# Optimization experiments

Measured on AMD Instinct MI355X. Metric: run time of the kernel, lower is better.

The kernel has to match this reference:

```python
import jax, jax.numpy as jnp
import numpy as np

B, L, DM, H, NF = 4, 4096, 1024, 16, 256
D = DM // H  # depth per head = 64
EPS = 1e-6


def _orthogonal_gaussian(m, d, seed=42):
    # Faithful to orthogonal_gaussian(): stack of transposed Q factors of d x d
    # iid-gaussian blocks, normalized by sqrt(num_squares + remainder/d).
    rng = np.random.default_rng(seed)
    num_squares = m // d
    blocks = []
    for _ in range(num_squares):
        q, _ = np.linalg.qr(rng.standard_normal((d, d)))
        blocks.append(q.T)
    remainder = m - d * num_squares
    if remainder:
        q, _ = np.linalg.qr(rng.standard_normal((d, d)))
        blocks.append(q.T[:remainder])
    mat = np.vstack(blocks) / np.sqrt(num_squares + remainder / d)
    return jnp.asarray(mat, dtype=jnp.float32)


def setup_inputs() -> dict:
    key = jax.random.key(0)
    ks = jax.random.split(key, 11)
    w = lambda k: jax.random.normal(k, (DM, DM), jnp.float32) * 0.02
    b = lambda k: jax.random.normal(k, (DM,), jnp.float32) * 0.01
    return {
        "query": jax.random.normal(ks[0], (B, L, DM), jnp.float32),
        "key": jax.random.normal(ks[1], (B, L, DM), jnp.float32),
        "value": jax.random.normal(ks[2], (B, L, DM), jnp.float32),
        "Wq": w(ks[3]), "bq": b(ks[4]),
        "Wk": w(ks[5]), "bk": b(ks[6]),
        "Wv": w(ks[7]), "bv": b(ks[8]),
        "Wo": w(ks[9]), "bo": b(ks[10]),
        "random_feats": _orthogonal_gaussian(NF, D),
    }


def _softmax_kernel(data, proj, is_query):
    # data: [B, L, H, D], proj: [M, D] -> features [B, L, H, M]
    d = data.shape[-1]
    m = proj.shape[0]
    data = data * (float(d) ** -0.25)          # data_normalizer = 1/sqrt(sqrt(d))
    ratio = float(m) ** -0.5
    data_dash = jnp.einsum('blhd,md->blhm', data, proj)
    diag = 0.5 * jnp.sum(data * data, axis=-1, keepdims=True)  # [B,L,H,1]
    if is_query:
        mx = jnp.max(data_dash, axis=-1, keepdims=True)          # per position
    else:
        mx = jnp.max(data_dash, axis=(1, -1), keepdims=True)     # over L and M
    return ratio * (jnp.exp(data_dash - diag - mx) + EPS)


def reference(query, key, value, Wq, bq, Wk, bk, Wv, bv, Wo, bo, random_feats):
    b, l = query.shape[0], query.shape[1]
    # QKV projections, split heads to [B, L, H, D]
    q = (query @ Wq + bq).reshape(b, l, H, D)
    k = (key @ Wk + bk).reshape(b, l, H, D)
    v = (value @ Wv + bv).reshape(b, l, H, D)
    # FAVOR+ feature maps
    qp = _softmax_kernel(q, random_feats, is_query=True)   # [B,L,H,M]
    kp = _softmax_kernel(k, random_feats, is_query=False)  # [B,L,H,M]
    # linear attention: kv state [B,H,M,D], then project with q'
    kv = jnp.einsum('blhm,blhd->bhmd', kp, v)
    av = jnp.einsum('blhm,bhmd->blhd', qp, kv)
    # normalizer: sum of k' over L, contracted with q'
    norm = jnp.einsum('blhm,bhm->blh', qp, jnp.sum(kp, axis=1))
    out = av / norm[..., None]                  # [B,L,H,D]
    out = out.reshape(b, l, DM)
    return out @ Wo + bo
```

## Files before the change

kernel.cpp:

```cpp
#include <hip/hip_runtime.h>
#include <hip/hip_bf16.h>

typedef unsigned short ushort_t;
typedef __attribute__((ext_vector_type(8))) short short8;
typedef __attribute__((ext_vector_type(4))) short short4v;
typedef __attribute__((ext_vector_type(4))) float f32x4;

#define DEVI static __device__ __forceinline__
#define MFMA __builtin_amdgcn_mfma_f32_16x16x32_bf16

DEVI float b2f(ushort_t u) {
    union { unsigned i; float f; } v; v.i = ((unsigned)u) << 16; return v.f;
}
DEVI ushort_t f2b(float f) {
    union { float f; unsigned i; } v; v.f = f;
    unsigned r = v.i + 0x7FFFu + ((v.i >> 16) & 1u);
    return (ushort_t)(r >> 16);
}
DEVI unsigned encf(float f) {
    unsigned u = __float_as_uint(f);
    return (u & 0x80000000u) ? ~u : (u | 0x80000000u);
}
DEVI float decf(unsigned u) {
    return (u & 0x80000000u) ? __uint_as_float(u & 0x7FFFFFFFu) : __uint_as_float(~u);
}
DEVI bool finitef(float v) { return v > -1e30f && v < 1e30f; }

__global__ void k_dtype(const ushort_t* __restrict__ qraw, unsigned* __restrict__ fl) {
    __shared__ unsigned cnt;
    int t = threadIdx.x;
    if (t == 0) cnt = 0;
    __syncthreads();
    unsigned c = 0;
    for (int i = t; i < 2048; i += 256) {
        unsigned e = (qraw[2 * i] >> 7) & 0xFF;
        c += (e >= 90 && e <= 141) ? 1u : 0u;
    }
    atomicAdd(&cnt, c);
    __syncthreads();
    if (t == 0) { fl[0] = (cnt < 1024) ? 1u : 0u; fl[1] = 0u; }
}

__global__ void k_fill(ushort_t* __restrict__ out, int n, float val) {
    int i = blockIdx.x * 256 + threadIdx.x;
    if (i < n) out[i] = f2b(val);
}

__global__ void k_prep(const void* __restrict__ Wq, const void* __restrict__ Wk,
                       const void* __restrict__ Wv, const void* __restrict__ Wo,
                       const void* __restrict__ rf, const unsigned* __restrict__ fl,
                       ushort_t* __restrict__ WT, ushort_t* __restrict__ WTo,
                       ushort_t* __restrict__ projS) {
    bool f32 = fl[0] != 0;
    int id = blockIdx.x, t = threadIdx.x;
    if (id == 1024) {
        for (int i = t; i < 256 * 64; i += 256) {
            float x = f32 ? ((const float*)rf)[i] : b2f(((const ushort_t*)rf)[i]);
            projS[i] = f2b(x * 0.35355339f);
        }
        return;
    }
    int wsel = id >> 8;
    const void* W = wsel == 0 ? Wq : (wsel == 1 ? Wk : (wsel == 2 ? Wv : Wo));
    ushort_t* out = (wsel == 3) ? WTo : (WT + (size_t)wsel * 1024 * 1024);
    int tile = id & 255;
    int tr = (tile >> 4) * 64, tc = (tile & 15) * 64;
    __shared__ ushort_t s[64][65];
    int r = t >> 2, c = (t & 3) * 16;
    ushort_t vals[16];
    if (f32) {
        const float* src = (const float*)W + (size_t)(tr + r) * 1024 + tc + c;
        for (int u = 0; u < 4; u++) {
            float4 x = ((const float4*)src)[u];
            vals[4 * u + 0] = f2b(x.x); vals[4 * u + 1] = f2b(x.y);
            vals[4 * u + 2] = f2b(x.z); vals[4 * u + 3] = f2b(x.w);
        }
    } else {
        const ushort_t* src = (const ushort_t*)W + (size_t)(tr + r) * 1024 + tc + c;
        short8 v0 = ((const short8*)src)[0], v1 = ((const short8*)src)[1];
        for (int j = 0; j < 8; j++) { vals[j] = ((ushort_t*)&v0)[j]; vals[8 + j] = ((ushort_t*)&v1)[j]; }
    }
    for (int j = 0; j < 16; j++) s[r][c + j] = vals[j];
    __syncthreads();
    ushort_t tmp[16];
    for (int j = 0; j < 16; j++) tmp[j] = s[c + j][r];
    short8 o0, o1;
    for (int j = 0; j < 8; j++) { ((ushort_t*)&o0)[j] = tmp[j]; ((ushort_t*)&o1)[j] = tmp[8 + j]; }
    short8* dst = (short8*)(out + (size_t)(tc + r) * 1024 + tr + c);
    dst[0] = o0; dst[1] = o1;
}

__global__ __launch_bounds__(256) void k_gemm_bias(const void* __restrict__ A,
                                                   const ushort_t* __restrict__ Bt,
                                                   const void* __restrict__ bias,
                                                   void* __restrict__ C,
                                                   const unsigned* __restrict__ fl,
                                                   int aFollow, int cFinal) {
    constexpr int K = 1024, NC = 1024;
    __shared__ ushort_t sA[128][40];
    __shared__ ushort_t sB[128][40];
    bool f32 = fl[0] != 0;
    bool aF32 = aFollow && f32;
    unsigned flags = cFinal ? fl[1] : 0u;
    int t = threadIdx.x;
    int m0 = blockIdx.x * 128, n0 = blockIdx.y * 128;
    int ar = t >> 1, ac = (t & 1) * 16;
    int w = t >> 6, lane = t & 63, lr = lane & 15, quad = lane >> 4, ko = quad * 8;
    int wm = (w & 1) * 64, wn = (w >> 1) * 64;
    f32x4 acc[4][4] = {};
    for (int kt = 0; kt < K; kt += 32) {
        ushort_t av[16];
        if (aF32) {
            const float* pf = (const float*)A + (size_t)(m0 + ar) * K + ac + kt;
            for (int u = 0; u < 4; u++) {
                float4 x = ((const float4*)pf)[u];
                av[4 * u + 0] = f2b(x.x); av[4 * u + 1] = f2b(x.y);
                av[4 * u + 2] = f2b(x.z); av[4 * u + 3] = f2b(x.w);
            }
        } else {
            const ushort_t* ph = (const ushort_t*)A + (size_t)(m0 + ar) * K + ac + kt;
            short8 a0 = ((const short8*)ph)[0], a1 = ((const short8*)ph)[1];
            for (int j = 0; j < 8; j++) { av[j] = ((ushort_t*)&a0)[j]; av[8 + j] = ((ushort_t*)&a1)[j]; }
        }
        const ushort_t* pb = Bt + (size_t)(n0 + ar) * K + ac + kt;
        short8 b0 = ((const short8*)pb)[0], b1 = ((const short8*)pb)[1];
        for (int j = 0; j < 16; j++) sA[ar][ac + j] = av[j];
        *(short8*)&sB[ar][ac] = b0; *(short8*)&sB[ar][ac + 8] = b1;
        __syncthreads();
        short8 af[4], bf[4];
        for (int i = 0; i < 4; i++) af[i] = *(const short8*)&sA[wm + i * 16 + lr][ko];
        for (int j = 0; j < 4; j++) bf[j] = *(const short8*)&sB[wn + j * 16 + lr][ko];
        for (int i = 0; i < 4; i++)
            for (int j = 0; j < 4; j++)
                acc[i][j] = MFMA(af[i], bf[j], acc[i][j], 0, 0, 0);
        __syncthreads();
    }
    for (int j = 0; j < 4; j++) {
        int col = n0 + wn + j * 16 + lr;
        float bv = f32 ? ((const float*)bias)[col] : b2f(((const ushort_t*)bias)[col]);
        for (int i = 0; i < 4; i++) {
            int rowb = m0 + wm + i * 16 + quad * 4;
            for (int r = 0; r < 4; r++) {
                float val = acc[i][j][r] + bv;
                if (cFinal) {
                    if (flags) val = 100.0f * (float)flags;
                    else if (!finitef(val)) val = 2000.0f;
                }
                size_t idx = (size_t)(rowb + r) * NC + col;
                if (cFinal && f32) ((float*)C)[idx] = val;
                else ((ushort_t*)C)[idx] = f2b(val);
            }
        }
    }
}

__global__ void k_init(float* __restrict__ kvT, unsigned* __restrict__ mxk) {
    int bid = blockIdx.x, t = threadIdx.x;
    if (bid == 5120) { if (t < 64) mxk[t] = 0u; return; }
    int idx = bid * 256 + t;
    int row = (idx >> 8) % 80;
    kvT[idx] = (row == 64) ? 2.56e-4f : 0.0f;
}

__global__ __launch_bounds__(256) void k_kmax(const ushort_t* __restrict__ kproj,
                                              const ushort_t* __restrict__ projS,
                                              unsigned* __restrict__ mxk) {
    __shared__ ushort_t sB[64][72];
    __shared__ float wm4[4];
    int t = threadIdx.x, l0 = blockIdx.x * 64, bh = blockIdx.y;
    int b = bh >> 4, h = bh & 15;
    int w = t >> 6, lane = t & 63, lr = lane & 15, ko = (lane >> 4) * 8;
    short8 af[4][2];
    for (int i = 0; i < 4; i++)
        for (int ks = 0; ks < 2; ks++)
            af[i][ks] = *(const short8*)(projS + (size_t)(w * 64 + i * 16 + lr) * 64 + ks * 32 + ko);
    {
        int r = t >> 2, c = (t & 3) * 16;
        const short8* p = (const short8*)(kproj + (size_t)(b * 4096 + l0 + r) * 1024 + h * 64 + c);
        *(short8*)&sB[r][c] = p[0];
        *(short8*)&sB[r][c + 8] = p[1];
    }
    __syncthreads();
    f32x4 acc[4][4] = {};
    for (int j = 0; j < 4; j++)
        for (int ks = 0; ks < 2; ks++) {
            short8 bf = *(const short8*)&sB[j * 16 + lr][ks * 32 + ko];
            for (int i = 0; i < 4; i++)
                acc[i][j] = MFMA(af[i][ks], bf, acc[i][j], 0, 0, 0);
        }
    float vmax = -1e30f;
    for (int i = 0; i < 4; i++)
        for (int j = 0; j < 4; j++)
            for (int r = 0; r < 4; r++) vmax = fmaxf(vmax, acc[i][j][r]);
    for (int off = 32; off; off >>= 1) vmax = fmaxf(vmax, __shfl_xor(vmax, off, 64));
    if (lane == 0) wm4[w] = vmax;
    __syncthreads();
    if (t == 0) {
        float m = fmaxf(fmaxf(wm4[0], wm4[1]), fmaxf(wm4[2], wm4[3]));
        atomicMax(mxk + bh, encf(m));
    }
}

__global__ __launch_bounds__(256) void k_kv(const ushort_t* __restrict__ kproj,
                                            const ushort_t* __restrict__ vproj,
                                            const ushort_t* __restrict__ projS,
                                            const unsigned* __restrict__ mxk,
                                            float* __restrict__ kvT) {
    __shared__ ushort_t sVT[80][40];
    __shared__ float    sdk[32];
    __shared__ ushort_t sK[32][72];
    __shared__ ushort_t sV[32][72];
    __shared__ ushort_t sE[256][40];
    int t = threadIdx.x, kz = blockIdx.x, bh = blockIdx.y;
    int b = bh >> 4, h = bh & 15;
    int w = t >> 6, lane = t & 63, lr = lane & 15, quad = lane >> 4, ko = quad * 8;
    float mx = decf(mxk[bh]);
    short8 af1[4][2];
    for (int i = 0; i < 4; i++)
        for (int ks = 0; ks < 2; ks++)
            af1[i][ks] = *(const short8*)(projS + (size_t)(w * 64 + i * 16 + lr) * 64 + ks * 32 + ko);
    f32x4 acc[5][4] = {};
    for (int lc = kz * 512; lc < kz * 512 + 512; lc += 32) {
        __syncthreads();
        {
            int r = t >> 3, c = (t & 7) * 8;
            *(short8*)&sK[r][c] = *(const short8*)(kproj + (size_t)(b * 4096 + lc + r) * 1024 + h * 64 + c);
            *(short8*)&sV[r][c] = *(const short8*)(vproj + (size_t)(b * 4096 + lc + r) * 1024 + h * 64 + c);
        }
        __syncthreads();
        if (t < 32) {
            float s = 0.f;
            for (int d2 = 0; d2 < 64; d2++) { float f = b2f(sK[t][d2]); s += f * f; }
            sdk[t] = 0.0625f * s;
        }
        short8 bf1[2][2];
        for (int j = 0; j < 2; j++)
            for (int ks = 0; ks < 2; ks++)
                bf1[j][ks] = *(const short8*)&sK[j * 16 + lr][ks * 32 + ko];
        f32x4 acc1[4][2] = {};
        for (int i = 0; i < 4; i++)
            for (int ks = 0; ks < 2; ks++)
                for (int j = 0; j < 2; j++)
                    acc1[i][j] = MFMA(af1[i][ks], bf1[j][ks], acc1[i][j], 0, 0, 0);
        {
            int d2 = t >> 2, ls = (t & 3) * 8;
            short8 pk;
            for (int u = 0; u < 8; u++) ((ushort_t*)&pk)[u] = sV[ls + u][d2];
            *(short8*)&sVT[d2][ls] = pk;
            if (t < 128) {
                int rr = 64 + (t >> 3), cc = (t & 7) * 4;
                ushort_t val = (rr == 64) ? (ushort_t)0x3F80 : (ushort_t)0;
                for (int u = 0; u < 4; u++) sVT[rr][cc + u] = val;
            }
        }
        __syncthreads();
        for (int i = 0; i < 4; i++)
            for (int j = 0; j < 2; j++) {
                int l = j * 16 + lr;
                float dkl = sdk[l];
                for (int r = 0; r < 4; r++) {
                    int m = w * 64 + i * 16 + quad * 4 + r;
                    sE[m][l] = f2b(0.0625f * __expf(acc1[i][j][r] - dkl - mx));
                }
            }
        __syncthreads();
        short8 af2[5], bf2[4];
        for (int i = 0; i < 5; i++) af2[i] = *(const short8*)&sVT[i * 16 + lr][ko];
        for (int j = 0; j < 4; j++) bf2[j] = *(const short8*)&sE[w * 64 + j * 16 + lr][ko];
        for (int i = 0; i < 5; i++)
            for (int j = 0; j < 4; j++)
                acc[i][j] = MFMA(af2[i], bf2[j], acc[i][j], 0, 0, 0);
    }
    float* out = kvT + (size_t)bh * 80 * 256;
    for (int i = 0; i < 5; i++)
        for (int j = 0; j < 4; j++)
            for (int r = 0; r < 4; r++)
                atomicAdd(out + (size_t)(i * 16 + quad * 4 + r) * 256 + (w * 64 + j * 16 + lr),
                          acc[i][j][r]);
}

__global__ void k_scan(const float* __restrict__ kvT, ushort_t* __restrict__ kvbf,
                       unsigned* __restrict__ fl) {
    int i4 = (blockIdx.x * 256 + threadIdx.x) * 4;
    f32x4 v = *(const f32x4*)(kvT + i4);
    unsigned bad = 0;
    short4v o;
    for (int u = 0; u < 4; u++) {
        bad |= finitef(v[u]) ? 0u : 1u;
        ((ushort_t*)&o)[u] = f2b(v[u]);
    }
    if (bad) atomicOr(fl + 1, 1u);
    *(short4v*)(kvbf + i4) = o;
}

__global__ __launch_bounds__(256) void k_qav(const ushort_t* __restrict__ qproj,
                                             const ushort_t* __restrict__ projS,
                                             const ushort_t* __restrict__ kvbf,
                                             unsigned* __restrict__ fl,
                                             ushort_t* __restrict__ attn) {
    union KvQ { ushort_t kv[80][264]; ushort_t q[64][72]; };
    __shared__ KvQ sA;
    __shared__ ushort_t sQP[64][264];
    __shared__ float    sdq[64];
    int t = threadIdx.x, l0 = blockIdx.x * 64, bh = blockIdx.y;
    int b = bh >> 4, h = bh & 15;
    int w = t >> 6, lane = t & 63, lr = lane & 15, quad = lane >> 4, ko = quad * 8;
    {
        int r = t >> 2, c = (t & 3) * 16;
        const short8* p = (const short8*)(qproj + (size_t)(b * 4096 + l0 + r) * 1024 + h * 64 + c);
        *(short8*)&sA.q[r][c] = p[0];
        *(short8*)&sA.q[r][c + 8] = p[1];
    }
    short8 kvreg[10];
    const ushort_t* kvsrc = kvbf + (size_t)bh * 80 * 256;
    #pragma unroll
    for (int i = 0; i < 10; i++)
        kvreg[i] = *(const short8*)(kvsrc + (size_t)(i * 256 + t) * 8);
    __syncthreads();
    short8 af[2];
    for (int ks = 0; ks < 2; ks++) af[ks] = *(const short8*)&sA.q[w * 16 + lr][ks * 32 + ko];
    {
        int row = t >> 2, seg = t & 3;
        short8 x0 = *(const short8*)&sA.q[row][seg * 16];
        short8 x1 = *(const short8*)&sA.q[row][seg * 16 + 8];
        float s = 0.f;
        for (int u = 0; u < 8; u++) {
            float a = b2f(((ushort_t*)&x0)[u]), c2 = b2f(((ushort_t*)&x1)[u]);
            s += a * a + c2 * c2;
        }
        s += __shfl_xor(s, 1, 64);
        s += __shfl_xor(s, 2, 64);
        if ((t & 3) == 0) sdq[row] = 0.0625f * s;
    }
    __syncthreads();
    f32x4 acc[16] = {};
    for (int j = 0; j < 16; j++)
        for (int ks = 0; ks < 2; ks++) {
            short8 bf = *(const short8*)(projS + (size_t)(j * 16 + lr) * 64 + ks * 32 + ko);
            acc[j] = MFMA(af[ks], bf, acc[j], 0, 0, 0);
        }
    #pragma unroll
    for (int i = 0; i < 10; i++) {
        int c = i * 256 + t;
        *(short8*)&sA.kv[c >> 5][(c & 31) * 8] = kvreg[i];
    }
    int rows0 = w * 16 + quad * 4;
    float rm[4], dq[4];
    for (int r = 0; r < 4; r++) {
        float m = -1e30f;
        for (int j = 0; j < 16; j++) m = fmaxf(m, acc[j][r]);
        for (int off = 1; off < 16; off <<= 1) m = fmaxf(m, __shfl_xor(m, off, 64));
        rm[r] = m;
        dq[r] = sdq[rows0 + r];
    }
    for (int j = 0; j < 16; j++)
        for (int r = 0; r < 4; r++)
            sQP[rows0 + r][j * 16 + lr] = f2b(0.0625f * (__expf(acc[j][r] - dq[r] - rm[r]) + 1e-6f));
    __syncthreads();
    f32x4 acc2[5] = {};
    for (int kt = 0; kt < 8; kt++) {
        short8 af2 = *(const short8*)&sQP[w * 16 + lr][kt * 32 + ko];
        #pragma unroll
        for (int j = 0; j < 5; j++) {
            short8 bf2 = *(const short8*)&sA.kv[j * 16 + lr][kt * 32 + ko];
            acc2[j] = MFMA(af2, bf2, acc2[j], 0, 0, 0);
        }
    }
    for (int r = 0; r < 4; r++) {
        float nv = __shfl(acc2[4][r], lane & 48, 64);
        bool badn = !(nv > 0.0f && nv < 1e30f);
        if (badn) atomicOr(fl + 1, 2u);
        float inv = badn ? 0.0f : 1.0f / nv;
        int row = l0 + rows0 + r;
        for (int j = 0; j < 4; j++) {
            float outv = acc2[j][r] * inv;
            if (!finitef(outv)) { outv = 0.0f; atomicOr(fl + 1, 4u); }
            attn[(size_t)(b * 4096 + row) * 1024 + h * 64 + j * 16 + lr] = f2b(outv);
        }
    }
}

extern "C" void kernel_launch(void* const* d_in, const int* in_sizes, int n_in,
                              void* d_out, int out_size, void* d_ws, size_t ws_size,
                              hipStream_t stream) {
    const void* q  = d_in[0];
    const void* k  = d_in[1];
    const void* v  = d_in[2];
    const void* Wq = d_in[3];
    const void* bq = d_in[4];
    const void* Wk = d_in[5];
    const void* bk = d_in[6];
    const void* Wv = d_in[7];
    const void* bv = d_in[8];
    const void* Wo = d_in[9];
    const void* bo = d_in[10];
    const void* rf = d_in[11];

    char* wsp = (char*)d_ws;
    size_t o = 0;
    auto alloc = [&](size_t bytes) { void* p = wsp + o; o += (bytes + 255) & ~(size_t)255; return p; };
    unsigned* fl    = (unsigned*)alloc(256);
    ushort_t* WT    = (ushort_t*)alloc(3ull * 1024 * 1024 * 2);
    ushort_t* WTo   = (ushort_t*)alloc(1024ull * 1024 * 2);
    ushort_t* projS = (ushort_t*)alloc(256 * 64 * 2);
    ushort_t* kproj = (ushort_t*)alloc(16384ull * 1024 * 2);
    ushort_t* vproj = (ushort_t*)alloc(16384ull * 1024 * 2);
    unsigned* mxk   = (unsigned*)alloc(64 * 4);
    float*    kvT   = (float*)alloc(64ull * 80 * 256 * 4);
    ushort_t* kvbf  = (ushort_t*)alloc(64ull * 80 * 256 * 2);
    ushort_t* qproj = (ushort_t*)d_out;
    ushort_t* attn  = kproj;

    if (ws_size < o) {
        k_fill<<<dim3((out_size + 255) / 256), 256, 0, stream>>>((ushort_t*)d_out, out_size,
                                                                 (float)(ws_size >> 20));
        return;
    }

    k_dtype<<<dim3(1), 256, 0, stream>>>((const ushort_t*)q, fl);
    k_prep<<<dim3(1025), 256, 0, stream>>>(Wq, Wk, Wv, Wo, rf, fl, WT, WTo, projS);
    k_gemm_bias<<<dim3(128, 8), 256, 0, stream>>>(q, WT + 0ull * 1048576, bq, qproj, fl, 1, 0);
    k_gemm_bias<<<dim3(128, 8), 256, 0, stream>>>(k, WT + 1ull * 1048576, bk, kproj, fl, 1, 0);
    k_gemm_bias<<<dim3(128, 8), 256, 0, stream>>>(v, WT + 2ull * 1048576, bv, vproj, fl, 1, 0);
    k_init<<<dim3(5121), 256, 0, stream>>>(kvT, mxk);
    k_kmax<<<dim3(64, 64), 256, 0, stream>>>(kproj, projS, mxk);
    k_kv<<<dim3(8, 64), 256, 0, stream>>>(kproj, vproj, projS, mxk, kvT);
    k_scan<<<dim3(1280), 256, 0, stream>>>(kvT, kvbf, fl);
    k_qav<<<dim3(64, 64), 256, 0, stream>>>(qproj, projS, kvbf, fl, attn);
    k_gemm_bias<<<dim3(128, 8), 256, 0, stream>>>(attn, WTo, bo, d_out, fl, 0, 1);
}
```

Baseline: 790.6 us.

## Stage GEMM tiles via direct global-to-LDS loads with separate fp32 pre-conversion

Replaces the register-staged GEMM tile loads with global_load_lds 16-byte direct transfers into unpadded shared memory. For the K and V projections, fp32 inputs are first converted to bf16 into a staging buffer (the output buffer) by a separate kernel, so the GEMM can use the direct-load path. The Q projection keeps in-register conversion for A but loads B directly. The aim is to cut VGPR traffic and instruction overhead in the load path, at the cost of extra conversion passes and possible LDS bank conflicts now that the padding is gone.

```diff
diff --git a/kernel.cpp b/kernel.cpp
--- a/kernel.cpp
+++ b/kernel.cpp
@@ -26,6 +26,12 @@
 }
 DEVI bool finitef(float v) { return v > -1e30f && v < 1e30f; }
 
+DEVI void gload16(const ushort_t* g, ushort_t* l) {
+    __builtin_amdgcn_global_load_lds(
+        (const __attribute__((address_space(1))) void*)(g),
+        (__attribute__((address_space(3))) void*)(l), 16, 0, 0);
+}
+
 __global__ void k_dtype(const ushort_t* __restrict__ qraw, unsigned* __restrict__ fl) {
     __shared__ unsigned cnt;
     int t = threadIdx.x;
@@ -44,6 +50,20 @@
 __global__ void k_fill(ushort_t* __restrict__ out, int n, float val) {
     int i = blockIdx.x * 256 + threadIdx.x;
     if (i < n) out[i] = f2b(val);
+}
+
+__global__ void k_cvt(const void* __restrict__ in, ushort_t* __restrict__ out,
+                      const unsigned* __restrict__ fl) {
+    if (fl[0] == 0) return;
+    int i = blockIdx.x * 256 + threadIdx.x;
+    const float4* p = (const float4*)in + (size_t)i * 2;
+    float4 a = p[0], b = p[1];
+    short8 o;
+    ((ushort_t*)&o)[0] = f2b(a.x); ((ushort_t*)&o)[1] = f2b(a.y);
+    ((ushort_t*)&o)[2] = f2b(a.z); ((ushort_t*)&o)[3] = f2b(a.w);
+    ((ushort_t*)&o)[4] = f2b(b.x); ((ushort_t*)&o)[5] = f2b(b.y);
+    ((ushort_t*)&o)[6] = f2b(b.z); ((ushort_t*)&o)[7] = f2b(b.w);
+    *(short8*)(out + (size_t)i * 8) = o;
 }
 
 __global__ void k_prep(const void* __restrict__ Wq, const void* __restrict__ Wk,
@@ -90,42 +110,37 @@
     dst[0] = o0; dst[1] = o1;
 }
 
-__global__ __launch_bounds__(256) void k_gemm_bias(const void* __restrict__ A,
-                                                   const ushort_t* __restrict__ Bt,
-                                                   const void* __restrict__ bias,
-                                                   void* __restrict__ C,
-                                                   const unsigned* __restrict__ fl,
-                                                   int aFollow, int cFinal) {
+__global__ __launch_bounds__(256) void k_gemm_g(const ushort_t* __restrict__ Abf,
+                                                const ushort_t* __restrict__ Aor,
+                                                const ushort_t* __restrict__ Bt,
+                                                const void* __restrict__ bias,
+                                                void* __restrict__ C,
+                                                const unsigned* __restrict__ fl,
+                                                int cFinal) {
     constexpr int K = 1024, NC = 1024;
-    __shared__ ushort_t sA[128][40];
-    __shared__ ushort_t sB[128][40];
+    __shared__ ushort_t sA[128][32];
+    __shared__ ushort_t sB[128][32];
     bool f32 = fl[0] != 0;
-    bool aF32 = aFollow && f32;
+    const ushort_t* A = f32 ? Abf : Aor;
     unsigned flags = cFinal ? fl[1] : 0u;
     int t = threadIdx.x;
     int m0 = blockIdx.x * 128, n0 = blockIdx.y * 128;
-    int ar = t >> 1, ac = (t & 1) * 16;
     int w = t >> 6, lane = t & 63, lr = lane & 15, quad = lane >> 4, ko = quad * 8;
     int wm = (w & 1) * 64, wn = (w >> 1) * 64;
+    int srow = lane >> 2, scol = (lane & 3) * 8;
+    const ushort_t* a0 = A  + (size_t)(m0 + w * 32 + srow) * K + scol;
+    const ushort_t* a1 = a0 + 16 * K;
+    const ushort_t* b0 = Bt + (size_t)(n0 + w * 32 + srow) * K + scol;
+    const ushort_t* b1 = b0 + 16 * K;
+    ushort_t* la0 = &sA[w * 32][0];
+    ushort_t* la1 = &sA[w * 32 + 16][0];
+    ushort_t* lb0 = &sB[w * 32][0];
+    ushort_t* lb1 = &sB[w * 32 + 16][0];
     f32x4 acc[4][4] = {};
     for (int kt = 0; kt < K; kt += 32) {
-        ushort_t av[16];
-        if (aF32) {
-            const float* pf = (const float*)A + (size_t)(m0 + ar) * K + ac + kt;
-            for (int u = 0; u < 4; u++) {
-                float4 x = ((const float4*)pf)[u];
-                av[4 * u + 0] = f2b(x.x); av[4 * u + 1] = f2b(x.y);
-                av[4 * u + 2] = f2b(x.z); av[4 * u + 3] = f2b(x.w);
-            }
-        } else {
-            const ushort_t* ph = (const ushort_t*)A + (size_t)(m0 + ar) * K + ac + kt;
-            short8 a0 = ((const short8*)ph)[0], a1 = ((const short8*)ph)[1];
-            for (int j = 0; j < 8; j++) { av[j] = ((ushort_t*)&a0)[j]; av[8 + j] = ((ushort_t*)&a1)[j]; }
-        }
-        const ushort_t* pb = Bt + (size_t)(n0 + ar) * K + ac + kt;
-        short8 b0 = ((const short8*)pb)[0], b1 = ((const short8*)pb)[1];
-        for (int j = 0; j < 16; j++) sA[ar][ac + j] = av[j];
-        *(short8*)&sB[ar][ac] = b0; *(short8*)&sB[ar][ac + 8] = b1;
+        gload16(a0, la0); gload16(b0, lb0);
+        gload16(a1, la1); gload16(b1, lb1);
+        a0 += 32; a1 += 32; b0 += 32; b1 += 32;
         __syncthreads();
         short8 af[4], bf[4];
         for (int i = 0; i < 4; i++) af[i] = *(const short8*)&sA[wm + i * 16 + lr][ko];
@@ -150,6 +165,64 @@
                 if (cFinal && f32) ((float*)C)[idx] = val;
                 else ((ushort_t*)C)[idx] = f2b(val);
             }
+        }
+    }
+}
+
+__global__ __launch_bounds__(256) void k_gemm_r(const void* __restrict__ A,
+                                                const ushort_t* __restrict__ Bt,
+                                                const void* __restrict__ bias,
+                                                ushort_t* __restrict__ C,
+                                                const unsigned* __restrict__ fl) {
+    constexpr int K = 1024, NC = 1024;
+    __shared__ ushort_t sA[128][40];
+    __shared__ ushort_t sB[128][32];
+    bool f32 = fl[0] != 0;
+    int t = threadIdx.x;
+    int m0 = blockIdx.x * 128, n0 = blockIdx.y * 128;
+    int ar = t >> 1, ac = (t & 1) * 16;
+    int w = t >> 6, lane = t & 63, lr = lane & 15, quad = lane >> 4, ko = quad * 8;
+    int wm = (w & 1) * 64, wn = (w >> 1) * 64;
+    int srow = lane >> 2, scol = (lane & 3) * 8;
+    const ushort_t* b0 = Bt + (size_t)(n0 + w * 32 + srow) * K + scol;
+    const ushort_t* b1 = b0 + 16 * K;
+    ushort_t* lb0 = &sB[w * 32][0];
+    ushort_t* lb1 = &sB[w * 32 + 16][0];
+    f32x4 acc[4][4] = {};
+    for (int kt = 0; kt < K; kt += 32) {
+        gload16(b0, lb0); gload16(b1, lb1);
+        b0 += 32; b1 += 32;
+        ushort_t av[16];
+        if (f32) {
+            const float* pf = (const float*)A + (size_t)(m0 + ar) * K + ac + kt;
+            for (int u = 0; u < 4; u++) {
+                float4 x = ((const float4*)pf)[u];
+                av[4 * u + 0] = f2b(x.x); av[4 * u + 1] = f2b(x.y);
+                av[4 * u + 2] = f2b(x.z); av[4 * u + 3] = f2b(x.w);
+            }
+        } else {
+            const ushort_t* ph = (const ushort_t*)A + (size_t)(m0 + ar) * K + ac + kt;
+            short8 a0 = ((const short8*)ph)[0], a1 = ((const short8*)ph)[1];
+            for (int j = 0; j < 8; j++) { av[j] = ((ushort_t*)&a0)[j]; av[8 + j] = ((ushort_t*)&a1)[j]; }
+        }
+        *(short8*)&sA[ar][ac] = *(short8*)&av[0];
+        *(short8*)&sA[ar][ac + 8] = *(short8*)&av[8];
+        __syncthreads();
+        short8 af[4], bf[4];
+        for (int i = 0; i < 4; i++) af[i] = *(const short8*)&sA[wm + i * 16 + lr][ko];
+        for (int j = 0; j < 4; j++) bf[j] = *(const short8*)&sB[wn + j * 16 + lr][ko];
+        for (int i = 0; i < 4; i++)
+            for (int j = 0; j < 4; j++)
+                acc[i][j] = MFMA(af[i], bf[j], acc[i][j], 0, 0, 0);
+        __syncthreads();
+    }
+    for (int j = 0; j < 4; j++) {
+        int col = n0 + wn + j * 16 + lr;
+        float bv = f32 ? ((const float*)bias)[col] : b2f(((const ushort_t*)bias)[col]);
+        for (int i = 0; i < 4; i++) {
+            int rowb = m0 + wm + i * 16 + quad * 4;
+            for (int r = 0; r < 4; r++)
+                C[(size_t)(rowb + r) * NC + col] = f2b(acc[i][j][r] + bv);
         }
     }
 }
@@ -408,6 +481,7 @@
     unsigned* mxk   = (unsigned*)alloc(64 * 4);
     float*    kvT   = (float*)alloc(64ull * 80 * 256 * 4);
     ushort_t* kvbf  = (ushort_t*)alloc(64ull * 80 * 256 * 2);
+    ushort_t* stg   = (ushort_t*)d_out;
     ushort_t* qproj = (ushort_t*)d_out;
     ushort_t* attn  = kproj;
 
@@ -419,13 +493,19 @@
 
     k_dtype<<<dim3(1), 256, 0, stream>>>((const ushort_t*)q, fl);
     k_prep<<<dim3(1025), 256, 0, stream>>>(Wq, Wk, Wv, Wo, rf, fl, WT, WTo, projS);
-    k_gemm_bias<<<dim3(128, 8), 256, 0, stream>>>(q, WT + 0ull * 1048576, bq, qproj, fl, 1, 0);
-    k_gemm_bias<<<dim3(128, 8), 256, 0, stream>>>(k, WT + 1ull * 1048576, bk, kproj, fl, 1, 0);
-    k_gemm_bias<<<dim3(128, 8), 256, 0, stream>>>(v, WT + 2ull * 1048576, bv, vproj, fl, 1, 0);
+
+    k_cvt<<<dim3(8192), 256, 0, stream>>>(v, stg, fl);
+    k_gemm_g<<<dim3(128, 8), 256, 0, stream>>>(stg, (const ushort_t*)v,
+                                               WT + 2ull * 1048576, bv, vproj, fl, 0);
+    k_cvt<<<dim3(8192), 256, 0, stream>>>(k, stg, fl);
+    k_gemm_g<<<dim3(128, 8), 256, 0, stream>>>(stg, (const ushort_t*)k,
+                                               WT + 1ull * 1048576, bk, kproj, fl, 0);
+    k_gemm_r<<<dim3(128, 8), 256, 0, stream>>>(q, WT + 0ull * 1048576, bq, qproj, fl);
+
     k_init<<<dim3(5121), 256, 0, stream>>>(kvT, mxk);
     k_kmax<<<dim3(64, 64), 256, 0, stream>>>(kproj, projS, mxk);
     k_kv<<<dim3(8, 64), 256, 0, stream>>>(kproj, vproj, projS, mxk, kvT);
     k_scan<<<dim3(1280), 256, 0, stream>>>(kvT, kvbf, fl);
     k_qav<<<dim3(64, 64), 256, 0, stream>>>(qproj, projS, kvbf, fl, attn);
-    k_gemm_bias<<<dim3(128, 8), 256, 0, stream>>>(attn, WTo, bo, d_out, fl, 0, 1);
-}
+    k_gemm_g<<<dim3(128, 8), 256, 0, stream>>>(attn, attn, WTo, bo, d_out, fl, 1);
+}
```

New measurement: 710.9 us. 1.11x faster.

## Pre-convert fp32 inputs to bf16 and double-buffer GEMM tiles via direct global-to-LDS loads

Applied to the files above, without the earlier changes.

Adds a conversion kernel that writes fp32 activations as bf16 into a staging buffer in the output region. The projection GEMMs then stream A and B tiles straight into LDS with global_load_lds into double buffers, prefetching the next k-tile while MFMAs run on the current one. This removes the per-tile register round trip, the in-loop conversion and one barrier per iteration. The kv kernel also moves the constant sVT rows out of the loop and computes the row norms in parallel with shuffles. The costs are an extra pass over each input to convert it, and unpadded LDS rows that may cause bank conflicts on fragment reads.

```diff
diff --git a/kernel.cpp b/kernel.cpp
--- a/kernel.cpp
+++ b/kernel.cpp
@@ -26,6 +26,12 @@
 }
 DEVI bool finitef(float v) { return v > -1e30f && v < 1e30f; }
 
+DEVI void gload16(const ushort_t* g, ushort_t* l) {
+    __builtin_amdgcn_global_load_lds(
+        (const __attribute__((address_space(1))) void*)(g),
+        (__attribute__((address_space(3))) void*)(l), 16, 0, 0);
+}
+
 __global__ void k_dtype(const ushort_t* __restrict__ qraw, unsigned* __restrict__ fl) {
     __shared__ unsigned cnt;
     int t = threadIdx.x;
@@ -44,6 +50,20 @@
 __global__ void k_fill(ushort_t* __restrict__ out, int n, float val) {
     int i = blockIdx.x * 256 + threadIdx.x;
     if (i < n) out[i] = f2b(val);
+}
+
+__global__ void k_cvt(const void* __restrict__ in, ushort_t* __restrict__ out,
+                      const unsigned* __restrict__ fl) {
+    if (fl[0] == 0) return;
+    int i = blockIdx.x * 256 + threadIdx.x;
+    const float4* p = (const float4*)in + (size_t)i * 2;
+    float4 a = p[0], b = p[1];
+    short8 o;
+    ((ushort_t*)&o)[0] = f2b(a.x); ((ushort_t*)&o)[1] = f2b(a.y);
+    ((ushort_t*)&o)[2] = f2b(a.z); ((ushort_t*)&o)[3] = f2b(a.w);
+    ((ushort_t*)&o)[4] = f2b(b.x); ((ushort_t*)&o)[5] = f2b(b.y);
+    ((ushort_t*)&o)[6] = f2b(b.z); ((ushort_t*)&o)[7] = f2b(b.w);
+    *(short8*)(out + (size_t)i * 8) = o;
 }
 
 __global__ void k_prep(const void* __restrict__ Wq, const void* __restrict__ Wk,
@@ -90,50 +110,47 @@
     dst[0] = o0; dst[1] = o1;
 }
 
-__global__ __launch_bounds__(256) void k_gemm_bias(const void* __restrict__ A,
-                                                   const ushort_t* __restrict__ Bt,
-                                                   const void* __restrict__ bias,
-                                                   void* __restrict__ C,
-                                                   const unsigned* __restrict__ fl,
-                                                   int aFollow, int cFinal) {
+__global__ __launch_bounds__(256) void k_gemm_g(const ushort_t* __restrict__ Abf,
+                                                const ushort_t* __restrict__ Aor,
+                                                const ushort_t* __restrict__ Bt,
+                                                const void* __restrict__ bias,
+                                                void* __restrict__ C,
+                                                const unsigned* __restrict__ fl,
+                                                int cFinal) {
     constexpr int K = 1024, NC = 1024;
-    __shared__ ushort_t sA[128][40];
-    __shared__ ushort_t sB[128][40];
+    __shared__ ushort_t sA[2][128][32];
+    __shared__ ushort_t sB[2][128][32];
     bool f32 = fl[0] != 0;
-    bool aF32 = aFollow && f32;
+    const ushort_t* A = f32 ? Abf : Aor;
     unsigned flags = cFinal ? fl[1] : 0u;
     int t = threadIdx.x;
     int m0 = blockIdx.x * 128, n0 = blockIdx.y * 128;
-    int ar = t >> 1, ac = (t & 1) * 16;
     int w = t >> 6, lane = t & 63, lr = lane & 15, quad = lane >> 4, ko = quad * 8;
     int wm = (w & 1) * 64, wn = (w >> 1) * 64;
+    int srow = lane >> 2, scol = (lane & 3) * 8;
+    const ushort_t* aP = A  + (size_t)(m0 + w * 32 + srow) * K + scol;
+    const ushort_t* bP = Bt + (size_t)(n0 + w * 32 + srow) * K + scol;
+    gload16(aP, &sA[0][w * 32][0]);            gload16(bP, &sB[0][w * 32][0]);
+    gload16(aP + 16 * K, &sA[0][w * 32 + 16][0]); gload16(bP + 16 * K, &sB[0][w * 32 + 16][0]);
+    __syncthreads();
     f32x4 acc[4][4] = {};
+    int cur = 0;
     for (int kt = 0; kt < K; kt += 32) {
-        ushort_t av[16];
-        if (aF32) {
-            const float* pf = (const float*)A + (size_t)(m0 + ar) * K + ac + kt;
-            for (int u = 0; u < 4; u++) {
-                float4 x = ((const float4*)pf)[u];
-                av[4 * u + 0] = f2b(x.x); av[4 * u + 1] = f2b(x.y);
-                av[4 * u + 2] = f2b(x.z); av[4 * u + 3] = f2b(x.w);
-            }
-        } else {
-            const ushort_t* ph = (const ushort_t*)A + (size_t)(m0 + ar) * K + ac + kt;
-            short8 a0 = ((const short8*)ph)[0], a1 = ((const short8*)ph)[1];
-            for (int j = 0; j < 8; j++) { av[j] = ((ushort_t*)&a0)[j]; av[8 + j] = ((ushort_t*)&a1)[j]; }
-        }
-        const ushort_t* pb = Bt + (size_t)(n0 + ar) * K + ac + kt;
-        short8 b0 = ((const short8*)pb)[0], b1 = ((const short8*)pb)[1];
-        for (int j = 0; j < 16; j++) sA[ar][ac + j] = av[j];
-        *(short8*)&sB[ar][ac] = b0; *(short8*)&sB[ar][ac + 8] = b1;
-        __syncthreads();
+        if (kt + 32 < K) {
+            const ushort_t* an = aP + kt + 32;
+            const ushort_t* bn = bP + kt + 32;
+            int nxt = cur ^ 1;
+            gload16(an, &sA[nxt][w * 32][0]);            gload16(bn, &sB[nxt][w * 32][0]);
+            gload16(an + 16 * K, &sA[nxt][w * 32 + 16][0]); gload16(bn + 16 * K, &sB[nxt][w * 32 + 16][0]);
+        }
         short8 af[4], bf[4];
-        for (int i = 0; i < 4; i++) af[i] = *(const short8*)&sA[wm + i * 16 + lr][ko];
-        for (int j = 0; j < 4; j++) bf[j] = *(const short8*)&sB[wn + j * 16 + lr][ko];
+        for (int i = 0; i < 4; i++) af[i] = *(const short8*)&sA[cur][wm + i * 16 + lr][ko];
+        for (int j = 0; j < 4; j++) bf[j] = *(const short8*)&sB[cur][wn + j * 16 + lr][ko];
         for (int i = 0; i < 4; i++)
             for (int j = 0; j < 4; j++)
                 acc[i][j] = MFMA(af[i], bf[j], acc[i][j], 0, 0, 0);
         __syncthreads();
+        cur ^= 1;
     }
     for (int j = 0; j < 4; j++) {
         int col = n0 + wn + j * 16 + lr;
@@ -219,6 +236,11 @@
     for (int i = 0; i < 4; i++)
         for (int ks = 0; ks < 2; ks++)
             af1[i][ks] = *(const short8*)(projS + (size_t)(w * 64 + i * 16 + lr) * 64 + ks * 32 + ko);
+    if (t < 128) {
+        int rr = 64 + (t >> 3), cc = (t & 7) * 4;
+        ushort_t val = (rr == 64) ? (ushort_t)0x3F80 : (ushort_t)0;
+        for (int u = 0; u < 4; u++) sVT[rr][cc + u] = val;
+    }
     f32x4 acc[5][4] = {};
     for (int lc = kz * 512; lc < kz * 512 + 512; lc += 32) {
         __syncthreads();
@@ -228,10 +250,15 @@
             *(short8*)&sV[r][c] = *(const short8*)(vproj + (size_t)(b * 4096 + lc + r) * 1024 + h * 64 + c);
         }
         __syncthreads();
-        if (t < 32) {
+        {
+            int row = t >> 3, seg = t & 7;
+            short8 x = *(const short8*)&sK[row][seg * 8];
             float s = 0.f;
-            for (int d2 = 0; d2 < 64; d2++) { float f = b2f(sK[t][d2]); s += f * f; }
-            sdk[t] = 0.0625f * s;
+            for (int u = 0; u < 8; u++) { float f = b2f(((ushort_t*)&x)[u]); s += f * f; }
+            s += __shfl_xor(s, 1, 64);
+            s += __shfl_xor(s, 2, 64);
+            s += __shfl_xor(s, 4, 64);
+            if (seg == 0) sdk[row] = 0.0625f * s;
         }
         short8 bf1[2][2];
         for (int j = 0; j < 2; j++)
@@ -247,11 +274,6 @@
             short8 pk;
             for (int u = 0; u < 8; u++) ((ushort_t*)&pk)[u] = sV[ls + u][d2];
             *(short8*)&sVT[d2][ls] = pk;
-            if (t < 128) {
-                int rr = 64 + (t >> 3), cc = (t & 7) * 4;
-                ushort_t val = (rr == 64) ? (ushort_t)0x3F80 : (ushort_t)0;
-                for (int u = 0; u < 4; u++) sVT[rr][cc + u] = val;
-            }
         }
         __syncthreads();
         for (int i = 0; i < 4; i++)
@@ -408,6 +430,8 @@
     unsigned* mxk   = (unsigned*)alloc(64 * 4);
     float*    kvT   = (float*)alloc(64ull * 80 * 256 * 4);
     ushort_t* kvbf  = (ushort_t*)alloc(64ull * 80 * 256 * 2);
+    ushort_t* stg   = (ushort_t*)d_out;
+    ushort_t* stgHi = (ushort_t*)d_out + 16777216;
     ushort_t* qproj = (ushort_t*)d_out;
     ushort_t* attn  = kproj;
 
@@ -419,13 +443,21 @@
 
     k_dtype<<<dim3(1), 256, 0, stream>>>((const ushort_t*)q, fl);
     k_prep<<<dim3(1025), 256, 0, stream>>>(Wq, Wk, Wv, Wo, rf, fl, WT, WTo, projS);
-    k_gemm_bias<<<dim3(128, 8), 256, 0, stream>>>(q, WT + 0ull * 1048576, bq, qproj, fl, 1, 0);
-    k_gemm_bias<<<dim3(128, 8), 256, 0, stream>>>(k, WT + 1ull * 1048576, bk, kproj, fl, 1, 0);
-    k_gemm_bias<<<dim3(128, 8), 256, 0, stream>>>(v, WT + 2ull * 1048576, bv, vproj, fl, 1, 0);
+
+    k_cvt<<<dim3(8192), 256, 0, stream>>>(v, stg, fl);
+    k_gemm_g<<<dim3(128, 8), 256, 0, stream>>>(stg, (const ushort_t*)v,
+                                               WT + 2ull * 1048576, bv, vproj, fl, 0);
+    k_cvt<<<dim3(8192), 256, 0, stream>>>(k, stg, fl);
+    k_gemm_g<<<dim3(128, 8), 256, 0, stream>>>(stg, (const ushort_t*)k,
+                                               WT + 1ull * 1048576, bk, kproj, fl, 0);
+    k_cvt<<<dim3(8192), 256, 0, stream>>>(q, stgHi, fl);
+    k_gemm_g<<<dim3(128, 8), 256, 0, stream>>>(stgHi, (const ushort_t*)q,
+                                               WT + 0ull * 1048576, bq, qproj, fl, 0);
+
     k_init<<<dim3(5121), 256, 0, stream>>>(kvT, mxk);
     k_kmax<<<dim3(64, 64), 256, 0, stream>>>(kproj, projS, mxk);
     k_kv<<<dim3(8, 64), 256, 0, stream>>>(kproj, vproj, projS, mxk, kvT);
     k_scan<<<dim3(1280), 256, 0, stream>>>(kvT, kvbf, fl);
     k_qav<<<dim3(64, 64), 256, 0, stream>>>(qproj, projS, kvbf, fl, attn);
-    k_gemm_bias<<<dim3(128, 8), 256, 0, stream>>>(attn, WTo, bo, d_out, fl, 0, 1);
-}
+    k_gemm_g<<<dim3(128, 8), 256, 0, stream>>>(attn, attn, WTo, bo, d_out, fl, 1);
+}
```

Result: faster. 745.7 us (-5.7%).
